# Kernel optimization log

Hardware: AMD Instinct MI355X
Metric: run time of the kernel (lower is better)

Reference implementation:

```python
import jax, jax.numpy as jnp
import numpy as np

N_NODES = 50000
N_EDGES = 800000
IN_DIM = 96
HID = 96
OUT_DIM = 32
N_GRAPHS = 256


def setup_inputs() -> dict:
    key = jax.random.key(0)
    ks = jax.random.split(key, 12)
    x = jax.random.normal(ks[0], (N_NODES, IN_DIM), dtype=jnp.float32)
    edge_index = jax.random.randint(ks[1], (2, N_EDGES), 0, N_NODES, dtype=jnp.int64)
    batch = jnp.sort(jax.random.randint(ks[2], (N_NODES,), 0, N_GRAPHS, dtype=jnp.int64))
    s = 1.0 / np.sqrt(HID)
    W1 = jax.random.normal(ks[3], (IN_DIM, HID), dtype=jnp.float32) * s
    W2 = jax.random.normal(ks[4], (HID, HID), dtype=jnp.float32) * s
    W3 = jax.random.normal(ks[5], (HID, HID), dtype=jnp.float32) * s
    fc_w = jax.random.normal(ks[6], (HID, OUT_DIM), dtype=jnp.float32) * s
    return {
        'x': x, 'edge_index': edge_index, 'batch': batch,
        'W1': W1, 'b1': jnp.zeros((HID,), jnp.float32),
        'W2': W2, 'b2': jnp.zeros((HID,), jnp.float32),
        'W3': W3, 'b3': jnp.zeros((HID,), jnp.float32),
        'fc_w': fc_w, 'fc_b': jnp.zeros((OUT_DIM,), jnp.float32),
    }


def _gcn_conv(h, row, col, norm, W, b, n_nodes):
    # linear transform first (PyG GCNConv), then normalized gather/scatter-add
    h = h @ W                                   # [N, F]
    msg = h[row] * norm[:, None]                # [E+N, F] gather + scale
    out = jax.ops.segment_sum(msg, col, num_segments=n_nodes)
    return out + b


def reference(x, edge_index, batch, W1, b1, W2, b2, W3, b3, fc_w, fc_b):
    n = x.shape[0]
    loop = jnp.arange(n, dtype=edge_index.dtype)
    row = jnp.concatenate([edge_index[0], loop])  # sources (with self-loops)
    col = jnp.concatenate([edge_index[1], loop])  # targets
    # symmetric normalization: deg over targets, norm = d^-1/2[row] * d^-1/2[col]
    deg = jax.ops.segment_sum(jnp.ones_like(col, dtype=x.dtype), col, num_segments=n)
    dis = jnp.where(deg > 0, jax.lax.rsqrt(deg), 0.0)
    norm = dis[row] * dis[col]

    h = jax.nn.relu(_gcn_conv(x, row, col, norm, W1, b1, n))
    h = jax.nn.relu(_gcn_conv(h, row, col, norm, W2, b2, n))
    h = jax.nn.relu(_gcn_conv(h, row, col, norm, W3, b3, n))

    # global_mean_pool over graph ids
    sums = jax.ops.segment_sum(h, batch, num_segments=N_GRAPHS)
    cnts = jax.ops.segment_sum(jnp.ones((n,), h.dtype), batch, num_segments=N_GRAPHS)
    pooled = sums / jnp.maximum(cnts, 1.0)[:, None]
    return pooled @ fc_w + fc_b
```

## Files before the change

kernel.cpp:

```cpp
#include <hip/hip_runtime.h>

#define NN 50000
#define NE 800000
#define F  96
#define FB 48
#define RB4 12
#define OD 32
#define NG 256
#define CAP 64
#define PROWS 21
#define SHARDS 8
#define SHARD_SZ 6250
#define PERSHARD 64
#define NWF 1152
#define RPB 64
#define TPB 256

typedef unsigned int u32;
typedef unsigned short u16;
typedef short short8 __attribute__((ext_vector_type(8)));
typedef float f32x4 __attribute__((ext_vector_type(4)));

static inline size_t align_up(size_t x) { return (x + 255) & ~(size_t)255; }

__device__ inline u32 f2bf_rne(float x) {
    u32 u = __float_as_uint(x);
    return (u + 0x7fffu + ((u >> 16) & 1u)) >> 16;
}
__device__ inline u32 packbf(float a, float b) {
    return f2bf_rne(a) | (f2bf_rne(b) << 16);
}
__device__ inline float bf_lo(u32 u) { return __uint_as_float(u << 16); }
__device__ inline float bf_hi(u32 u) { return __uint_as_float(u & 0xffff0000u); }

__global__ __launch_bounds__(256) void k_pack(const int* __restrict__ src,
                                              const int* __restrict__ tgt,
                                              uint4* __restrict__ ep4) {
    int c = blockIdx.x * 256 + threadIdx.x;
    if (c >= NE / 4) return;
    int4 s4 = reinterpret_cast<const int4*>(src)[c];
    int4 t4 = reinterpret_cast<const int4*>(tgt)[c];
    ep4[c] = make_uint4(((u32)t4.x << 16) | (u32)s4.x, ((u32)t4.y << 16) | (u32)s4.y,
                        ((u32)t4.z << 16) | (u32)s4.z, ((u32)t4.w << 16) | (u32)s4.w);
}

__global__ __launch_bounds__(256) void k_fillb(const uint4* __restrict__ ep4,
                                               int* __restrict__ cnt,
                                               u16* __restrict__ bucket) {
    int shard = blockIdx.x & (SHARDS - 1);
    int sb    = blockIdx.x >> 3;
    int lo    = shard * SHARD_SZ;
    int hi    = lo + SHARD_SZ;
    const int nchunk = NE / 4;
    for (int c = sb * 256 + threadIdx.x; c < nchunk; c += PERSHARD * 256) {
        uint4 p = ep4[c];
        int t0 = p.x >> 16, s0 = p.x & 0xffff;
        int t1 = p.y >> 16, s1 = p.y & 0xffff;
        int t2 = p.z >> 16, s2 = p.z & 0xffff;
        int t3 = p.w >> 16, s3 = p.w & 0xffff;
        if (t0 >= lo && t0 < hi) {
            int q = atomicAdd(&cnt[t0], 1);
            if (q < CAP) bucket[t0 * CAP + q] = (u16)s0;
        }
        if (t1 >= lo && t1 < hi) {
            int q = atomicAdd(&cnt[t1], 1);
            if (q < CAP) bucket[t1 * CAP + q] = (u16)s1;
        }
        if (t2 >= lo && t2 < hi) {
            int q = atomicAdd(&cnt[t2], 1);
            if (q < CAP) bucket[t2 * CAP + q] = (u16)s2;
        }
        if (t3 >= lo && t3 < hi) {
            int q = atomicAdd(&cnt[t3], 1);
            if (q < CAP) bucket[t3 * CAP + q] = (u16)s3;
        }
    }
}

__global__ __launch_bounds__(256) void k_cvt(const float4* __restrict__ x4,
                                             const int* __restrict__ cnt,
                                             float* __restrict__ dis,
                                             uint4* __restrict__ rb4) {
    int i = blockIdx.x * 256 + threadIdx.x;
    if (i >= NN * RB4) return;
    int v   = i / RB4;
    int sub = i - v * RB4;
    float dv = rsqrtf((float)(cnt[v] + 1));
    if (sub == 0) dis[v] = dv;
    float4 f0 = x4[(size_t)i * 2];
    float4 f1 = x4[(size_t)i * 2 + 1];
    rb4[i] = make_uint4(packbf(dv * f0.x, dv * f0.y), packbf(dv * f0.z, dv * f0.w),
                        packbf(dv * f1.x, dv * f1.y), packbf(dv * f1.z, dv * f1.w));
}

__global__ __launch_bounds__(256) void k_wprep3(const float* __restrict__ W1,
                                                const float* __restrict__ W2,
                                                const float* __restrict__ W3,
                                                uint4* __restrict__ wf) {
    int e = blockIdx.x * 256 + threadIdx.x;
    if (e >= 3 * NWF) return;
    int wi = e / NWF;
    int f  = e - wi * NWF;
    const float* W = (wi == 0) ? W1 : ((wi == 1) ? W2 : W3);
    int n  = f & 15;
    int t1 = f >> 4;
    int quad = t1 & 3;
    int t2 = t1 >> 2;
    int kc = t2 % 3;
    int ct = t2 / 3;
    int k  = kc * 32 + quad * 8;
    int col = ct * 16 + n;
    u32 w0 = packbf(W[(k + 0) * F + col], W[(k + 1) * F + col]);
    u32 w1 = packbf(W[(k + 2) * F + col], W[(k + 3) * F + col]);
    u32 w2 = packbf(W[(k + 4) * F + col], W[(k + 5) * F + col]);
    u32 w3 = packbf(W[(k + 6) * F + col], W[(k + 7) * F + col]);
    wf[e] = make_uint4(w0, w1, w2, w3);
}

__global__ __launch_bounds__(TPB) void k_layer(const uint4* __restrict__ rprev,
                                               const uint4* __restrict__ wfragG,
                                               const int* __restrict__ cnt,
                                               const u16* __restrict__ bucket,
                                               const float* __restrict__ dis,
                                               const float* __restrict__ bias,
                                               const int last,
                                               u16* __restrict__ rnext) {
    __shared__ uint4 atile[RPB * 13];
    int tid = threadIdx.x;
    int r0 = blockIdx.x * RPB;

    const u32* hb = reinterpret_cast<const u32*>(rprev);

#pragma unroll
    for (int it = 0; it < 3; ++it) {
        int slot = it * TPB + tid;
        int ln  = slot / 12;
        int sub = slot - ln * 12;
        int v = r0 + ln;
        uint4 res = make_uint4(0u, 0u, 0u, 0u);
        if (v < NN) {
            int co = sub * 4;
            uint4 hv = *reinterpret_cast<const uint4*>(&hb[(size_t)v * FB + co]);
            float a0 = bf_lo(hv.x), a1 = bf_hi(hv.x);
            float a2 = bf_lo(hv.y), a3 = bf_hi(hv.y);
            float a4 = bf_lo(hv.z), a5 = bf_hi(hv.z);
            float a6 = bf_lo(hv.w), a7 = bf_hi(hv.w);

            int deg = cnt[v];
            if (deg > CAP) deg = CAP;
            const u16* bkt = &bucket[v * CAP];
            int e = 0;
            for (; e + 7 < deg; e += 8) {
                uint4 b8 = *reinterpret_cast<const uint4*>(&bkt[e]);
                int s0 = b8.x & 0xffff, s1 = b8.x >> 16;
                int s2 = b8.y & 0xffff, s3 = b8.y >> 16;
                int s4 = b8.z & 0xffff, s5 = b8.z >> 16;
                int s6 = b8.w & 0xffff, s7 = b8.w >> 16;
                uint4 g0 = *reinterpret_cast<const uint4*>(&hb[(size_t)s0 * FB + co]);
                uint4 g1 = *reinterpret_cast<const uint4*>(&hb[(size_t)s1 * FB + co]);
                uint4 g2 = *reinterpret_cast<const uint4*>(&hb[(size_t)s2 * FB + co]);
                uint4 g3 = *reinterpret_cast<const uint4*>(&hb[(size_t)s3 * FB + co]);
                uint4 g4 = *reinterpret_cast<const uint4*>(&hb[(size_t)s4 * FB + co]);
                uint4 g5 = *reinterpret_cast<const uint4*>(&hb[(size_t)s5 * FB + co]);
                uint4 g6 = *reinterpret_cast<const uint4*>(&hb[(size_t)s6 * FB + co]);
                uint4 g7 = *reinterpret_cast<const uint4*>(&hb[(size_t)s7 * FB + co]);
                a0 += bf_lo(g0.x) + bf_lo(g1.x) + bf_lo(g2.x) + bf_lo(g3.x)
                    + bf_lo(g4.x) + bf_lo(g5.x) + bf_lo(g6.x) + bf_lo(g7.x);
                a1 += bf_hi(g0.x) + bf_hi(g1.x) + bf_hi(g2.x) + bf_hi(g3.x)
                    + bf_hi(g4.x) + bf_hi(g5.x) + bf_hi(g6.x) + bf_hi(g7.x);
                a2 += bf_lo(g0.y) + bf_lo(g1.y) + bf_lo(g2.y) + bf_lo(g3.y)
                    + bf_lo(g4.y) + bf_lo(g5.y) + bf_lo(g6.y) + bf_lo(g7.y);
                a3 += bf_hi(g0.y) + bf_hi(g1.y) + bf_hi(g2.y) + bf_hi(g3.y)
                    + bf_hi(g4.y) + bf_hi(g5.y) + bf_hi(g6.y) + bf_hi(g7.y);
                a4 += bf_lo(g0.z) + bf_lo(g1.z) + bf_lo(g2.z) + bf_lo(g3.z)
                    + bf_lo(g4.z) + bf_lo(g5.z) + bf_lo(g6.z) + bf_lo(g7.z);
                a5 += bf_hi(g0.z) + bf_hi(g1.z) + bf_hi(g2.z) + bf_hi(g3.z)
                    + bf_hi(g4.z) + bf_hi(g5.z) + bf_hi(g6.z) + bf_hi(g7.z);
                a6 += bf_lo(g0.w) + bf_lo(g1.w) + bf_lo(g2.w) + bf_lo(g3.w)
                    + bf_lo(g4.w) + bf_lo(g5.w) + bf_lo(g6.w) + bf_lo(g7.w);
                a7 += bf_hi(g0.w) + bf_hi(g1.w) + bf_hi(g2.w) + bf_hi(g3.w)
                    + bf_hi(g4.w) + bf_hi(g5.w) + bf_hi(g6.w) + bf_hi(g7.w);
            }
            for (; e + 3 < deg; e += 4) {
                uint2 b4 = *reinterpret_cast<const uint2*>(&bkt[e]);
                int s0 = b4.x & 0xffff, s1 = b4.x >> 16;
                int s2 = b4.y & 0xffff, s3 = b4.y >> 16;
                uint4 g0 = *reinterpret_cast<const uint4*>(&hb[(size_t)s0 * FB + co]);
                uint4 g1 = *reinterpret_cast<const uint4*>(&hb[(size_t)s1 * FB + co]);
                uint4 g2 = *reinterpret_cast<const uint4*>(&hb[(size_t)s2 * FB + co]);
                uint4 g3 = *reinterpret_cast<const uint4*>(&hb[(size_t)s3 * FB + co]);
                a0 += bf_lo(g0.x) + bf_lo(g1.x) + bf_lo(g2.x) + bf_lo(g3.x);
                a1 += bf_hi(g0.x) + bf_hi(g1.x) + bf_hi(g2.x) + bf_hi(g3.x);
                a2 += bf_lo(g0.y) + bf_lo(g1.y) + bf_lo(g2.y) + bf_lo(g3.y);
                a3 += bf_hi(g0.y) + bf_hi(g1.y) + bf_hi(g2.y) + bf_hi(g3.y);
                a4 += bf_lo(g0.z) + bf_lo(g1.z) + bf_lo(g2.z) + bf_lo(g3.z);
                a5 += bf_hi(g0.z) + bf_hi(g1.z) + bf_hi(g2.z) + bf_hi(g3.z);
                a6 += bf_lo(g0.w) + bf_lo(g1.w) + bf_lo(g2.w) + bf_lo(g3.w);
                a7 += bf_hi(g0.w) + bf_hi(g1.w) + bf_hi(g2.w) + bf_hi(g3.w);
            }
            for (; e < deg; ++e) {
                int s = bkt[e];
                uint4 g = *reinterpret_cast<const uint4*>(&hb[(size_t)s * FB + co]);
                a0 += bf_lo(g.x); a1 += bf_hi(g.x);
                a2 += bf_lo(g.y); a3 += bf_hi(g.y);
                a4 += bf_lo(g.z); a5 += bf_hi(g.z);
                a6 += bf_lo(g.w); a7 += bf_hi(g.w);
            }
            float dv = dis[v];
            res = make_uint4(packbf(dv * a0, dv * a1), packbf(dv * a2, dv * a3),
                             packbf(dv * a4, dv * a5), packbf(dv * a6, dv * a7));
        }
        atile[ln * 13 + sub] = res;
    }
    __syncthreads();

    int wave = tid >> 6;
    int lane = tid & 63;
    int m    = lane & 15;
    int quad = lane >> 4;
    int arow = wave * 16 + m;

    short8 a0 = *reinterpret_cast<const short8*>(&atile[arow * 13 + 0 * 4 + quad]);
    short8 a1 = *reinterpret_cast<const short8*>(&atile[arow * 13 + 1 * 4 + quad]);
    short8 a2 = *reinterpret_cast<const short8*>(&atile[arow * 13 + 2 * 4 + quad]);

    f32x4 acc[6];
#pragma unroll
    for (int ct = 0; ct < 6; ++ct) acc[ct] = (f32x4)(0.0f);
#pragma unroll
    for (int ct = 0; ct < 6; ++ct) {
        short8 b0 = *reinterpret_cast<const short8*>(&wfragG[((ct * 3 + 0) * 4 + quad) * 16 + m]);
        short8 b1 = *reinterpret_cast<const short8*>(&wfragG[((ct * 3 + 1) * 4 + quad) * 16 + m]);
        short8 b2 = *reinterpret_cast<const short8*>(&wfragG[((ct * 3 + 2) * 4 + quad) * 16 + m]);
        acc[ct] = __builtin_amdgcn_mfma_f32_16x16x32_bf16(a0, b0, acc[ct], 0, 0, 0);
        acc[ct] = __builtin_amdgcn_mfma_f32_16x16x32_bf16(a1, b1, acc[ct], 0, 0, 0);
        acc[ct] = __builtin_amdgcn_mfma_f32_16x16x32_bf16(a2, b2, acc[ct], 0, 0, 0);
    }

    int rbase = r0 + wave * 16 + quad * 4;
    float dr[4];
#pragma unroll
    for (int r = 0; r < 4; ++r) {
        int row = rbase + r;
        dr[r] = (row < NN) ? (last ? 1.0f : dis[row]) : 0.0f;
    }
#pragma unroll
    for (int ct = 0; ct < 6; ++ct) {
        float bb = bias[ct * 16 + m];
#pragma unroll
        for (int r = 0; r < 4; ++r) {
            int row = rbase + r;
            if (row < NN) {
                float h = fmaxf(acc[ct][r] + bb, 0.0f);
                rnext[(size_t)row * F + ct * 16 + m] = (u16)f2bf_rne(h * dr[r]);
            }
        }
    }
}

__device__ inline int lower_bound_i(const int* __restrict__ a, int n, int key) {
    int lo = 0, hi = n;
    while (lo < hi) {
        int mid = (lo + hi) >> 1;
        if (a[mid] < key) lo = mid + 1; else hi = mid;
    }
    return lo;
}

__global__ __launch_bounds__(512) void k_poolfc(const uint2* __restrict__ hb2,
                                                const int* __restrict__ batch,
                                                const float* __restrict__ fcw,
                                                const float* __restrict__ fcb,
                                                float* __restrict__ out) {
    __shared__ int range[2];
    __shared__ float4 part[PROWS][24];
    __shared__ float pl[F];
    int g = blockIdx.x;
    int t = threadIdx.x;
    if (t == 0) range[0] = lower_bound_i(batch, NN, g);
    if (t == 1) range[1] = lower_bound_i(batch, NN, g + 1);
    __syncthreads();
    int lo = range[0], hi = range[1];
    int row = t / 24;
    int sub = t - row * 24;
    if (row < PROWS) {
        float4 acc = make_float4(0.f, 0.f, 0.f, 0.f);
        for (int v = lo + row; v < hi; v += PROWS) {
            uint2 xv = hb2[(size_t)v * 24 + sub];
            acc.x += bf_lo(xv.x); acc.y += bf_hi(xv.x);
            acc.z += bf_lo(xv.y); acc.w += bf_hi(xv.y);
        }
        part[row][sub] = acc;
    }
    __syncthreads();
    if (t < 24) {
        float4 s = part[0][t];
        for (int r = 1; r < PROWS; ++r) {
            float4 p = part[r][t];
            s.x += p.x; s.y += p.y; s.z += p.z; s.w += p.w;
        }
        float inv = 1.0f / fmaxf((float)(hi - lo), 1.0f);
        pl[t * 4 + 0] = s.x * inv;
        pl[t * 4 + 1] = s.y * inv;
        pl[t * 4 + 2] = s.z * inv;
        pl[t * 4 + 3] = s.w * inv;
    }
    __syncthreads();
    if (t < OD) {
        float acc = 0.0f;
        for (int f = 0; f < F; ++f) acc += pl[f] * fcw[f * OD + t];
        out[g * OD + t] = acc + fcb[t];
    }
}

extern "C" void kernel_launch(void* const* d_in, const int* in_sizes, int n_in,
                              void* d_out, int out_size, void* d_ws, size_t ws_size,
                              hipStream_t stream) {
    (void)in_sizes; (void)n_in; (void)out_size; (void)ws_size;
    const float* x    = (const float*)d_in[0];
    const int*   ei   = (const int*)d_in[1];
    const int*   batc = (const int*)d_in[2];
    const float* W1   = (const float*)d_in[3];
    const float* b1   = (const float*)d_in[4];
    const float* W2   = (const float*)d_in[5];
    const float* b2   = (const float*)d_in[6];
    const float* W3   = (const float*)d_in[7];
    const float* b3   = (const float*)d_in[8];
    const float* fcw  = (const float*)d_in[9];
    const float* fcb  = (const float*)d_in[10];
    float* out = (float*)d_out;

    const int* src = ei;
    const int* tgt = ei + NE;

    char* ws = (char*)d_ws;
    int*    cnt    = (int*)ws;    ws += align_up((size_t)NN * 4);
    float*  dis    = (float*)ws;  ws += align_up((size_t)NN * 4);
    u16*    bucket = (u16*)ws;    ws += align_up((size_t)NN * CAP * 2);
    u32*    ep     = (u32*)ws;    ws += align_up((size_t)NE * 4);
    u32*    rA     = (u32*)ws;    ws += align_up((size_t)NN * FB * 4);
    u32*    rB     = (u32*)ws;    ws += align_up((size_t)NN * FB * 4);
    uint4*  wfrag3 = (uint4*)ws;  ws += align_up((size_t)3 * NWF * 16);

    const int B = 256;
    const int cvt_grid   = (NN * RB4 + B - 1) / B;
    const int wprep_grid = (3 * NWF + B - 1) / B;
    const int pack_grid  = (NE / 4 + B - 1) / B;
    const int layer_grid = (NN + RPB - 1) / RPB;

    (void)hipMemsetAsync(cnt, 0, (size_t)NN * 4, stream);
    k_pack  <<<pack_grid, B, 0, stream>>>(src, tgt, (uint4*)ep);
    k_fillb <<<SHARDS * PERSHARD, B, 0, stream>>>((const uint4*)ep, cnt, bucket);
    k_wprep3<<<wprep_grid, B, 0, stream>>>(W1, W2, W3, wfrag3);
    k_cvt   <<<cvt_grid, B, 0, stream>>>((const float4*)x, cnt, dis, (uint4*)rA);

    k_layer<<<layer_grid, TPB, 0, stream>>>((const uint4*)rA, wfrag3 + 0 * NWF,
                                            cnt, bucket, dis, b1, 0, (u16*)rB);
    k_layer<<<layer_grid, TPB, 0, stream>>>((const uint4*)rB, wfrag3 + 1 * NWF,
                                            cnt, bucket, dis, b2, 0, (u16*)rA);
    k_layer<<<layer_grid, TPB, 0, stream>>>((const uint4*)rA, wfrag3 + 2 * NWF,
                                            cnt, bucket, dis, b3, 1, (u16*)rB);

    k_poolfc<<<NG, 512, 0, stream>>>((const uint2*)rB, batc, fcw, fcb, out);
}
```

Before: 242.5 us.

## Split fused layer kernel into separate aggregation and MFMA matmul kernels

Replaces the fused per-layer kernel (gather-aggregate into LDS, then MFMA against the weights) with two kernels: a flat gather kernel writing bf16 aggregates to a global scratch buffer, and a matmul kernel that reads them back for the MFMA step. This is meant to decouple the irregular gather from the matmul and raise occupancy for the gather (launch bounds 256,4, no LDS), avoiding the barrier and LDS footprint that limited the fused version. In exchange it adds an extra global write and read of an N x 96 bf16 buffer per layer plus three more kernel launches.

```diff
diff --git a/kernel.cpp b/kernel.cpp
--- a/kernel.cpp
+++ b/kernel.cpp
@@ -14,7 +14,7 @@
 #define PERSHARD 64
 #define NWF 1152
 #define RPB 64
-#define TPB 256
+#define ASLOTS (NN * 12)
 
 typedef unsigned int u32;
 typedef unsigned short u16;
@@ -117,112 +117,111 @@
     wf[e] = make_uint4(w0, w1, w2, w3);
 }
 
-__global__ __launch_bounds__(TPB) void k_layer(const uint4* __restrict__ rprev,
-                                               const uint4* __restrict__ wfragG,
-                                               const int* __restrict__ cnt,
-                                               const u16* __restrict__ bucket,
-                                               const float* __restrict__ dis,
-                                               const float* __restrict__ bias,
-                                               const int last,
-                                               u16* __restrict__ rnext) {
-    __shared__ uint4 atile[RPB * 13];
-    int tid = threadIdx.x;
-    int r0 = blockIdx.x * RPB;
-
+__global__ __launch_bounds__(256, 4) void k_agg(const uint4* __restrict__ rprev,
+                                                const int* __restrict__ cnt,
+                                                const u16* __restrict__ bucket,
+                                                const float* __restrict__ dis,
+                                                uint4* __restrict__ aggb) {
+    int slot = blockIdx.x * 256 + threadIdx.x;
+    if (slot >= ASLOTS) return;
+    int v   = slot / 12;
+    int sub = slot - v * 12;
+    int co  = sub * 4;
     const u32* hb = reinterpret_cast<const u32*>(rprev);
 
-#pragma unroll
-    for (int it = 0; it < 3; ++it) {
-        int slot = it * TPB + tid;
-        int ln  = slot / 12;
-        int sub = slot - ln * 12;
-        int v = r0 + ln;
-        uint4 res = make_uint4(0u, 0u, 0u, 0u);
-        if (v < NN) {
-            int co = sub * 4;
-            uint4 hv = *reinterpret_cast<const uint4*>(&hb[(size_t)v * FB + co]);
-            float a0 = bf_lo(hv.x), a1 = bf_hi(hv.x);
-            float a2 = bf_lo(hv.y), a3 = bf_hi(hv.y);
-            float a4 = bf_lo(hv.z), a5 = bf_hi(hv.z);
-            float a6 = bf_lo(hv.w), a7 = bf_hi(hv.w);
-
-            int deg = cnt[v];
-            if (deg > CAP) deg = CAP;
-            const u16* bkt = &bucket[v * CAP];
-            int e = 0;
-            for (; e + 7 < deg; e += 8) {
-                uint4 b8 = *reinterpret_cast<const uint4*>(&bkt[e]);
-                int s0 = b8.x & 0xffff, s1 = b8.x >> 16;
-                int s2 = b8.y & 0xffff, s3 = b8.y >> 16;
-                int s4 = b8.z & 0xffff, s5 = b8.z >> 16;
-                int s6 = b8.w & 0xffff, s7 = b8.w >> 16;
-                uint4 g0 = *reinterpret_cast<const uint4*>(&hb[(size_t)s0 * FB + co]);
-                uint4 g1 = *reinterpret_cast<const uint4*>(&hb[(size_t)s1 * FB + co]);
-                uint4 g2 = *reinterpret_cast<const uint4*>(&hb[(size_t)s2 * FB + co]);
-                uint4 g3 = *reinterpret_cast<const uint4*>(&hb[(size_t)s3 * FB + co]);
-                uint4 g4 = *reinterpret_cast<const uint4*>(&hb[(size_t)s4 * FB + co]);
-                uint4 g5 = *reinterpret_cast<const uint4*>(&hb[(size_t)s5 * FB + co]);
-                uint4 g6 = *reinterpret_cast<const uint4*>(&hb[(size_t)s6 * FB + co]);
-                uint4 g7 = *reinterpret_cast<const uint4*>(&hb[(size_t)s7 * FB + co]);
-                a0 += bf_lo(g0.x) + bf_lo(g1.x) + bf_lo(g2.x) + bf_lo(g3.x)
-                    + bf_lo(g4.x) + bf_lo(g5.x) + bf_lo(g6.x) + bf_lo(g7.x);
-                a1 += bf_hi(g0.x) + bf_hi(g1.x) + bf_hi(g2.x) + bf_hi(g3.x)
-                    + bf_hi(g4.x) + bf_hi(g5.x) + bf_hi(g6.x) + bf_hi(g7.x);
-                a2 += bf_lo(g0.y) + bf_lo(g1.y) + bf_lo(g2.y) + bf_lo(g3.y)
-                    + bf_lo(g4.y) + bf_lo(g5.y) + bf_lo(g6.y) + bf_lo(g7.y);
-                a3 += bf_hi(g0.y) + bf_hi(g1.y) + bf_hi(g2.y) + bf_hi(g3.y)
-                    + bf_hi(g4.y) + bf_hi(g5.y) + bf_hi(g6.y) + bf_hi(g7.y);
-                a4 += bf_lo(g0.z) + bf_lo(g1.z) + bf_lo(g2.z) + bf_lo(g3.z)
-                    + bf_lo(g4.z) + bf_lo(g5.z) + bf_lo(g6.z) + bf_lo(g7.z);
-                a5 += bf_hi(g0.z) + bf_hi(g1.z) + bf_hi(g2.z) + bf_hi(g3.z)
-                    + bf_hi(g4.z) + bf_hi(g5.z) + bf_hi(g6.z) + bf_hi(g7.z);
-                a6 += bf_lo(g0.w) + bf_lo(g1.w) + bf_lo(g2.w) + bf_lo(g3.w)
-                    + bf_lo(g4.w) + bf_lo(g5.w) + bf_lo(g6.w) + bf_lo(g7.w);
-                a7 += bf_hi(g0.w) + bf_hi(g1.w) + bf_hi(g2.w) + bf_hi(g3.w)
-                    + bf_hi(g4.w) + bf_hi(g5.w) + bf_hi(g6.w) + bf_hi(g7.w);
-            }
-            for (; e + 3 < deg; e += 4) {
-                uint2 b4 = *reinterpret_cast<const uint2*>(&bkt[e]);
-                int s0 = b4.x & 0xffff, s1 = b4.x >> 16;
-                int s2 = b4.y & 0xffff, s3 = b4.y >> 16;
-                uint4 g0 = *reinterpret_cast<const uint4*>(&hb[(size_t)s0 * FB + co]);
-                uint4 g1 = *reinterpret_cast<const uint4*>(&hb[(size_t)s1 * FB + co]);
-                uint4 g2 = *reinterpret_cast<const uint4*>(&hb[(size_t)s2 * FB + co]);
-                uint4 g3 = *reinterpret_cast<const uint4*>(&hb[(size_t)s3 * FB + co]);
-                a0 += bf_lo(g0.x) + bf_lo(g1.x) + bf_lo(g2.x) + bf_lo(g3.x);
-                a1 += bf_hi(g0.x) + bf_hi(g1.x) + bf_hi(g2.x) + bf_hi(g3.x);
-                a2 += bf_lo(g0.y) + bf_lo(g1.y) + bf_lo(g2.y) + bf_lo(g3.y);
-                a3 += bf_hi(g0.y) + bf_hi(g1.y) + bf_hi(g2.y) + bf_hi(g3.y);
-                a4 += bf_lo(g0.z) + bf_lo(g1.z) + bf_lo(g2.z) + bf_lo(g3.z);
-                a5 += bf_hi(g0.z) + bf_hi(g1.z) + bf_hi(g2.z) + bf_hi(g3.z);
-                a6 += bf_lo(g0.w) + bf_lo(g1.w) + bf_lo(g2.w) + bf_lo(g3.w);
-                a7 += bf_hi(g0.w) + bf_hi(g1.w) + bf_hi(g2.w) + bf_hi(g3.w);
-            }
-            for (; e < deg; ++e) {
-                int s = bkt[e];
-                uint4 g = *reinterpret_cast<const uint4*>(&hb[(size_t)s * FB + co]);
-                a0 += bf_lo(g.x); a1 += bf_hi(g.x);
-                a2 += bf_lo(g.y); a3 += bf_hi(g.y);
-                a4 += bf_lo(g.z); a5 += bf_hi(g.z);
-                a6 += bf_lo(g.w); a7 += bf_hi(g.w);
-            }
-            float dv = dis[v];
-            res = make_uint4(packbf(dv * a0, dv * a1), packbf(dv * a2, dv * a3),
-                             packbf(dv * a4, dv * a5), packbf(dv * a6, dv * a7));
-        }
-        atile[ln * 13 + sub] = res;
-    }
-    __syncthreads();
-
+    uint4 hv = *reinterpret_cast<const uint4*>(&hb[(size_t)v * FB + co]);
+    float a0 = bf_lo(hv.x), a1 = bf_hi(hv.x);
+    float a2 = bf_lo(hv.y), a3 = bf_hi(hv.y);
+    float a4 = bf_lo(hv.z), a5 = bf_hi(hv.z);
+    float a6 = bf_lo(hv.w), a7 = bf_hi(hv.w);
+
+    int deg = cnt[v];
+    if (deg > CAP) deg = CAP;
+    const u16* bkt = &bucket[v * CAP];
+    int e = 0;
+    for (; e + 7 < deg; e += 8) {
+        uint4 b8 = *reinterpret_cast<const uint4*>(&bkt[e]);
+        int s0 = b8.x & 0xffff, s1 = b8.x >> 16;
+        int s2 = b8.y & 0xffff, s3 = b8.y >> 16;
+        int s4 = b8.z & 0xffff, s5 = b8.z >> 16;
+        int s6 = b8.w & 0xffff, s7 = b8.w >> 16;
+        uint4 g0 = *reinterpret_cast<const uint4*>(&hb[(size_t)s0 * FB + co]);
+        uint4 g1 = *reinterpret_cast<const uint4*>(&hb[(size_t)s1 * FB + co]);
+        uint4 g2 = *reinterpret_cast<const uint4*>(&hb[(size_t)s2 * FB + co]);
+        uint4 g3 = *reinterpret_cast<const uint4*>(&hb[(size_t)s3 * FB + co]);
+        uint4 g4 = *reinterpret_cast<const uint4*>(&hb[(size_t)s4 * FB + co]);
+        uint4 g5 = *reinterpret_cast<const uint4*>(&hb[(size_t)s5 * FB + co]);
+        uint4 g6 = *reinterpret_cast<const uint4*>(&hb[(size_t)s6 * FB + co]);
+        uint4 g7 = *reinterpret_cast<const uint4*>(&hb[(size_t)s7 * FB + co]);
+        a0 += bf_lo(g0.x) + bf_lo(g1.x) + bf_lo(g2.x) + bf_lo(g3.x)
+            + bf_lo(g4.x) + bf_lo(g5.x) + bf_lo(g6.x) + bf_lo(g7.x);
+        a1 += bf_hi(g0.x) + bf_hi(g1.x) + bf_hi(g2.x) + bf_hi(g3.x)
+            + bf_hi(g4.x) + bf_hi(g5.x) + bf_hi(g6.x) + bf_hi(g7.x);
+        a2 += bf_lo(g0.y) + bf_lo(g1.y) + bf_lo(g2.y) + bf_lo(g3.y)
+            + bf_lo(g4.y) + bf_lo(g5.y) + bf_lo(g6.y) + bf_lo(g7.y);
+        a3 += bf_hi(g0.y) + bf_hi(g1.y) + bf_hi(g2.y) + bf_hi(g3.y)
+            + bf_hi(g4.y) + bf_hi(g5.y) + bf_hi(g6.y) + bf_hi(g7.y);
+        a4 += bf_lo(g0.z) + bf_lo(g1.z) + bf_lo(g2.z) + bf_lo(g3.z)
+            + bf_lo(g4.z) + bf_lo(g5.z) + bf_lo(g6.z) + bf_lo(g7.z);
+        a5 += bf_hi(g0.z) + bf_hi(g1.z) + bf_hi(g2.z) + bf_hi(g3.z)
+            + bf_hi(g4.z) + bf_hi(g5.z) + bf_hi(g6.z) + bf_hi(g7.z);
+        a6 += bf_lo(g0.w) + bf_lo(g1.w) + bf_lo(g2.w) + bf_lo(g3.w)
+            + bf_lo(g4.w) + bf_lo(g5.w) + bf_lo(g6.w) + bf_lo(g7.w);
+        a7 += bf_hi(g0.w) + bf_hi(g1.w) + bf_hi(g2.w) + bf_hi(g3.w)
+            + bf_hi(g4.w) + bf_hi(g5.w) + bf_hi(g6.w) + bf_hi(g7.w);
+    }
+    for (; e + 3 < deg; e += 4) {
+        uint2 b4 = *reinterpret_cast<const uint2*>(&bkt[e]);
+        int s0 = b4.x & 0xffff, s1 = b4.x >> 16;
+        int s2 = b4.y & 0xffff, s3 = b4.y >> 16;
+        uint4 g0 = *reinterpret_cast<const uint4*>(&hb[(size_t)s0 * FB + co]);
+        uint4 g1 = *reinterpret_cast<const uint4*>(&hb[(size_t)s1 * FB + co]);
+        uint4 g2 = *reinterpret_cast<const uint4*>(&hb[(size_t)s2 * FB + co]);
+        uint4 g3 = *reinterpret_cast<const uint4*>(&hb[(size_t)s3 * FB + co]);
+        a0 += bf_lo(g0.x) + bf_lo(g1.x) + bf_lo(g2.x) + bf_lo(g3.x);
+        a1 += bf_hi(g0.x) + bf_hi(g1.x) + bf_hi(g2.x) + bf_hi(g3.x);
+        a2 += bf_lo(g0.y) + bf_lo(g1.y) + bf_lo(g2.y) + bf_lo(g3.y);
+        a3 += bf_hi(g0.y) + bf_hi(g1.y) + bf_hi(g2.y) + bf_hi(g3.y);
+        a4 += bf_lo(g0.z) + bf_lo(g1.z) + bf_lo(g2.z) + bf_lo(g3.z);
+        a5 += bf_hi(g0.z) + bf_hi(g1.z) + bf_hi(g2.z) + bf_hi(g3.z);
+        a6 += bf_lo(g0.w) + bf_lo(g1.w) + bf_lo(g2.w) + bf_lo(g3.w);
+        a7 += bf_hi(g0.w) + bf_hi(g1.w) + bf_hi(g2.w) + bf_hi(g3.w);
+    }
+    for (; e < deg; ++e) {
+        int s = bkt[e];
+        uint4 g = *reinterpret_cast<const uint4*>(&hb[(size_t)s * FB + co]);
+        a0 += bf_lo(g.x); a1 += bf_hi(g.x);
+        a2 += bf_lo(g.y); a3 += bf_hi(g.y);
+        a4 += bf_lo(g.z); a5 += bf_hi(g.z);
+        a6 += bf_lo(g.w); a7 += bf_hi(g.w);
+    }
+    float dv = dis[v];
+    aggb[slot] = make_uint4(packbf(dv * a0, dv * a1), packbf(dv * a2, dv * a3),
+                            packbf(dv * a4, dv * a5), packbf(dv * a6, dv * a7));
+}
+
+__global__ __launch_bounds__(256) void k_mm(const uint4* __restrict__ aggb,
+                                            const uint4* __restrict__ wfragG,
+                                            const float* __restrict__ dis,
+                                            const float* __restrict__ bias,
+                                            const int last,
+                                            u16* __restrict__ rnext) {
+    int tid  = threadIdx.x;
+    int r0   = blockIdx.x * RPB;
     int wave = tid >> 6;
     int lane = tid & 63;
     int m    = lane & 15;
     int quad = lane >> 4;
-    int arow = wave * 16 + m;
-
-    short8 a0 = *reinterpret_cast<const short8*>(&atile[arow * 13 + 0 * 4 + quad]);
-    short8 a1 = *reinterpret_cast<const short8*>(&atile[arow * 13 + 1 * 4 + quad]);
-    short8 a2 = *reinterpret_cast<const short8*>(&atile[arow * 13 + 2 * 4 + quad]);
+    int arow = r0 + wave * 16 + m;
+    bool rv  = arow < NN;
+
+    size_t abase = (size_t)arow * 12;
+    short8 a0 = (short8)(short)0, a1 = (short8)(short)0, a2 = (short8)(short)0;
+    if (rv) {
+        a0 = *reinterpret_cast<const short8*>(&aggb[abase + 0 * 4 + quad]);
+        a1 = *reinterpret_cast<const short8*>(&aggb[abase + 1 * 4 + quad]);
+        a2 = *reinterpret_cast<const short8*>(&aggb[abase + 2 * 4 + quad]);
+    }
 
     f32x4 acc[6];
 #pragma unroll
@@ -340,13 +339,15 @@
     u32*    ep     = (u32*)ws;    ws += align_up((size_t)NE * 4);
     u32*    rA     = (u32*)ws;    ws += align_up((size_t)NN * FB * 4);
     u32*    rB     = (u32*)ws;    ws += align_up((size_t)NN * FB * 4);
+    u32*    rC     = (u32*)ws;    ws += align_up((size_t)NN * FB * 4);
     uint4*  wfrag3 = (uint4*)ws;  ws += align_up((size_t)3 * NWF * 16);
 
     const int B = 256;
     const int cvt_grid   = (NN * RB4 + B - 1) / B;
     const int wprep_grid = (3 * NWF + B - 1) / B;
     const int pack_grid  = (NE / 4 + B - 1) / B;
-    const int layer_grid = (NN + RPB - 1) / RPB;
+    const int agg_grid   = (ASLOTS + B - 1) / B;
+    const int mm_grid    = (NN + RPB - 1) / RPB;
 
     (void)hipMemsetAsync(cnt, 0, (size_t)NN * 4, stream);
     k_pack  <<<pack_grid, B, 0, stream>>>(src, tgt, (uint4*)ep);
@@ -354,12 +355,14 @@
     k_wprep3<<<wprep_grid, B, 0, stream>>>(W1, W2, W3, wfrag3);
     k_cvt   <<<cvt_grid, B, 0, stream>>>((const float4*)x, cnt, dis, (uint4*)rA);
 
-    k_layer<<<layer_grid, TPB, 0, stream>>>((const uint4*)rA, wfrag3 + 0 * NWF,
-                                            cnt, bucket, dis, b1, 0, (u16*)rB);
-    k_layer<<<layer_grid, TPB, 0, stream>>>((const uint4*)rB, wfrag3 + 1 * NWF,
-                                            cnt, bucket, dis, b2, 0, (u16*)rA);
-    k_layer<<<layer_grid, TPB, 0, stream>>>((const uint4*)rA, wfrag3 + 2 * NWF,
-                                            cnt, bucket, dis, b3, 1, (u16*)rB);
+    k_agg<<<agg_grid, B, 0, stream>>>((const uint4*)rA, cnt, bucket, dis, (uint4*)rC);
+    k_mm <<<mm_grid, B, 0, stream>>>((const uint4*)rC, wfrag3 + 0 * NWF, dis, b1, 0, (u16*)rB);
+
+    k_agg<<<agg_grid, B, 0, stream>>>((const uint4*)rB, cnt, bucket, dis, (uint4*)rC);
+    k_mm <<<mm_grid, B, 0, stream>>>((const uint4*)rC, wfrag3 + 1 * NWF, dis, b2, 0, (u16*)rA);
+
+    k_agg<<<agg_grid, B, 0, stream>>>((const uint4*)rA, cnt, bucket, dis, (uint4*)rC);
+    k_mm <<<mm_grid, B, 0, stream>>>((const uint4*)rC, wfrag3 + 2 * NWF, dis, b3, 1, (u16*)rB);
 
     k_poolfc<<<NG, 512, 0, stream>>>((const uint2*)rB, batc, fcw, fcb, out);
 }
```

New measurement: 249.8 us. 3.0% more time.

## Process nodes in degree-sorted order and fuse setup kernels

Applied to the files above, without the earlier changes.

Adds a counting sort of nodes by in-degree (a histogram built in the prep kernel plus a scatter kernel that builds a permutation). Each layer block then handles rows through that permutation, so warps gather similar numbers of neighbours and divergence and load imbalance shrink. The memset, edge pack and weight-prep steps are merged into one kernel to cut launches. In exchange it adds a permutation indirection, scattered output writes, and global atomics during the histogram and scatter.

```diff
diff --git a/kernel.cpp b/kernel.cpp
--- a/kernel.cpp
+++ b/kernel.cpp
@@ -33,15 +33,42 @@
 __device__ inline float bf_lo(u32 u) { return __uint_as_float(u << 16); }
 __device__ inline float bf_hi(u32 u) { return __uint_as_float(u & 0xffff0000u); }
 
-__global__ __launch_bounds__(256) void k_pack(const int* __restrict__ src,
-                                              const int* __restrict__ tgt,
-                                              uint4* __restrict__ ep4) {
-    int c = blockIdx.x * 256 + threadIdx.x;
-    if (c >= NE / 4) return;
-    int4 s4 = reinterpret_cast<const int4*>(src)[c];
-    int4 t4 = reinterpret_cast<const int4*>(tgt)[c];
-    ep4[c] = make_uint4(((u32)t4.x << 16) | (u32)s4.x, ((u32)t4.y << 16) | (u32)s4.y,
-                        ((u32)t4.z << 16) | (u32)s4.z, ((u32)t4.w << 16) | (u32)s4.w);
+__global__ __launch_bounds__(256) void k_prep1(const int* __restrict__ src,
+                                               const int* __restrict__ tgt,
+                                               const float* __restrict__ W1,
+                                               const float* __restrict__ W2,
+                                               const float* __restrict__ W3,
+                                               uint4* __restrict__ wf,
+                                               int* __restrict__ cnt,
+                                               int* __restrict__ histcur,
+                                               uint4* __restrict__ ep4) {
+    int g = blockIdx.x * 256 + threadIdx.x;
+    if (g < NN) cnt[g] = 0;
+    if (g < 2 * (CAP + 1)) histcur[g] = 0;
+    if (g < NE / 4) {
+        int4 s4 = reinterpret_cast<const int4*>(src)[g];
+        int4 t4 = reinterpret_cast<const int4*>(tgt)[g];
+        ep4[g] = make_uint4(((u32)t4.x << 16) | (u32)s4.x, ((u32)t4.y << 16) | (u32)s4.y,
+                            ((u32)t4.z << 16) | (u32)s4.z, ((u32)t4.w << 16) | (u32)s4.w);
+    }
+    if (g < 3 * NWF) {
+        int wi = g / NWF;
+        int f  = g - wi * NWF;
+        const float* W = (wi == 0) ? W1 : ((wi == 1) ? W2 : W3);
+        int n  = f & 15;
+        int t1 = f >> 4;
+        int quad = t1 & 3;
+        int t2 = t1 >> 2;
+        int kc = t2 % 3;
+        int ct = t2 / 3;
+        int k  = kc * 32 + quad * 8;
+        int col = ct * 16 + n;
+        u32 w0 = packbf(W[(k + 0) * F + col], W[(k + 1) * F + col]);
+        u32 w1 = packbf(W[(k + 2) * F + col], W[(k + 3) * F + col]);
+        u32 w2 = packbf(W[(k + 4) * F + col], W[(k + 5) * F + col]);
+        u32 w3 = packbf(W[(k + 6) * F + col], W[(k + 7) * F + col]);
+        wf[g] = make_uint4(w0, w1, w2, w3);
+    }
 }
 
 __global__ __launch_bounds__(256) void k_fillb(const uint4* __restrict__ ep4,
@@ -77,44 +104,46 @@
     }
 }
 
-__global__ __launch_bounds__(256) void k_cvt(const float4* __restrict__ x4,
-                                             const int* __restrict__ cnt,
-                                             float* __restrict__ dis,
-                                             uint4* __restrict__ rb4) {
+__global__ __launch_bounds__(256) void k_prep2(const float4* __restrict__ x4,
+                                               const int* __restrict__ cnt,
+                                               float* __restrict__ dis,
+                                               uint4* __restrict__ rb4,
+                                               int* __restrict__ histcur) {
     int i = blockIdx.x * 256 + threadIdx.x;
     if (i >= NN * RB4) return;
     int v   = i / RB4;
     int sub = i - v * RB4;
     float dv = rsqrtf((float)(cnt[v] + 1));
-    if (sub == 0) dis[v] = dv;
+    if (sub == 0) {
+        dis[v] = dv;
+        int d = cnt[v];
+        if (d > CAP) d = CAP;
+        atomicAdd(&histcur[d], 1);
+    }
     float4 f0 = x4[(size_t)i * 2];
     float4 f1 = x4[(size_t)i * 2 + 1];
     rb4[i] = make_uint4(packbf(dv * f0.x, dv * f0.y), packbf(dv * f0.z, dv * f0.w),
                         packbf(dv * f1.x, dv * f1.y), packbf(dv * f1.z, dv * f1.w));
 }
 
-__global__ __launch_bounds__(256) void k_wprep3(const float* __restrict__ W1,
-                                                const float* __restrict__ W2,
-                                                const float* __restrict__ W3,
-                                                uint4* __restrict__ wf) {
-    int e = blockIdx.x * 256 + threadIdx.x;
-    if (e >= 3 * NWF) return;
-    int wi = e / NWF;
-    int f  = e - wi * NWF;
-    const float* W = (wi == 0) ? W1 : ((wi == 1) ? W2 : W3);
-    int n  = f & 15;
-    int t1 = f >> 4;
-    int quad = t1 & 3;
-    int t2 = t1 >> 2;
-    int kc = t2 % 3;
-    int ct = t2 / 3;
-    int k  = kc * 32 + quad * 8;
-    int col = ct * 16 + n;
-    u32 w0 = packbf(W[(k + 0) * F + col], W[(k + 1) * F + col]);
-    u32 w1 = packbf(W[(k + 2) * F + col], W[(k + 3) * F + col]);
-    u32 w2 = packbf(W[(k + 4) * F + col], W[(k + 5) * F + col]);
-    u32 w3 = packbf(W[(k + 6) * F + col], W[(k + 7) * F + col]);
-    wf[e] = make_uint4(w0, w1, w2, w3);
+__global__ __launch_bounds__(256) void k_scatter(const int* __restrict__ cnt,
+                                                 int* __restrict__ histcur,
+                                                 int* __restrict__ perm) {
+    __shared__ int sstart[CAP + 1];
+    int t = threadIdx.x;
+    if (t <= CAP) {
+        int s = 0;
+        for (int d2 = CAP; d2 > t; --d2) s += histcur[d2];
+        sstart[t] = s;
+    }
+    __syncthreads();
+    int v = blockIdx.x * 256 + t;
+    if (v < NN) {
+        int d = cnt[v];
+        if (d > CAP) d = CAP;
+        int pos = sstart[d] + atomicAdd(&histcur[(CAP + 1) + d], 1);
+        perm[pos] = v;
+    }
 }
 
 __global__ __launch_bounds__(TPB) void k_layer(const uint4* __restrict__ rprev,
@@ -123,6 +152,7 @@
                                                const u16* __restrict__ bucket,
                                                const float* __restrict__ dis,
                                                const float* __restrict__ bias,
+                                               const int* __restrict__ perm,
                                                const int last,
                                                u16* __restrict__ rnext) {
     __shared__ uint4 atile[RPB * 13];
@@ -136,9 +166,10 @@
         int slot = it * TPB + tid;
         int ln  = slot / 12;
         int sub = slot - ln * 12;
-        int v = r0 + ln;
+        int idx = r0 + ln;
         uint4 res = make_uint4(0u, 0u, 0u, 0u);
-        if (v < NN) {
+        if (idx < NN) {
+            int v = perm[idx];
             int co = sub * 4;
             uint4 hv = *reinterpret_cast<const uint4*>(&hb[(size_t)v * FB + co]);
             float a0 = bf_lo(hv.x), a1 = bf_hi(hv.x);
@@ -239,10 +270,17 @@
 
     int rbase = r0 + wave * 16 + quad * 4;
     float dr[4];
+    int prow[4];
 #pragma unroll
     for (int r = 0; r < 4; ++r) {
         int row = rbase + r;
-        dr[r] = (row < NN) ? (last ? 1.0f : dis[row]) : 0.0f;
+        if (row < NN) {
+            prow[r] = perm[row];
+            dr[r] = last ? 1.0f : dis[prow[r]];
+        } else {
+            prow[r] = 0;
+            dr[r] = 0.0f;
+        }
     }
 #pragma unroll
     for (int ct = 0; ct < 6; ++ct) {
@@ -252,7 +290,7 @@
             int row = rbase + r;
             if (row < NN) {
                 float h = fmaxf(acc[ct][r] + bb, 0.0f);
-                rnext[(size_t)row * F + ct * 16 + m] = (u16)f2bf_rne(h * dr[r]);
+                rnext[(size_t)prow[r] * F + ct * 16 + m] = (u16)f2bf_rne(h * dr[r]);
             }
         }
     }
@@ -341,25 +379,28 @@
     u32*    rA     = (u32*)ws;    ws += align_up((size_t)NN * FB * 4);
     u32*    rB     = (u32*)ws;    ws += align_up((size_t)NN * FB * 4);
     uint4*  wfrag3 = (uint4*)ws;  ws += align_up((size_t)3 * NWF * 16);
+    int*    perm   = (int*)ws;    ws += align_up((size_t)NN * 4);
+    int*    histc  = (int*)ws;    ws += align_up((size_t)2 * (CAP + 1) * 4);
 
     const int B = 256;
-    const int cvt_grid   = (NN * RB4 + B - 1) / B;
-    const int wprep_grid = (3 * NWF + B - 1) / B;
-    const int pack_grid  = (NE / 4 + B - 1) / B;
+    const int prep1_grid = (NE / 4 + B - 1) / B;
+    const int prep2_grid = (NN * RB4 + B - 1) / B;
+    const int scat_grid  = (NN + B - 1) / B;
     const int layer_grid = (NN + RPB - 1) / RPB;
 
-    (void)hipMemsetAsync(cnt, 0, (size_t)NN * 4, stream);
-    k_pack  <<<pack_grid, B, 0, stream>>>(src, tgt, (uint4*)ep);
-    k_fillb <<<SHARDS * PERSHARD, B, 0, stream>>>((const uint4*)ep, cnt, bucket);
-    k_wprep3<<<wprep_grid, B, 0, stream>>>(W1, W2, W3, wfrag3);
-    k_cvt   <<<cvt_grid, B, 0, stream>>>((const float4*)x, cnt, dis, (uint4*)rA);
+    k_prep1  <<<prep1_grid, B, 0, stream>>>(src, tgt, W1, W2, W3, wfrag3,
+                                            cnt, histc, (uint4*)ep);
+    k_fillb  <<<SHARDS * PERSHARD, B, 0, stream>>>((const uint4*)ep, cnt, bucket);
+    k_prep2  <<<prep2_grid, B, 0, stream>>>((const float4*)x, cnt, dis,
+                                            (uint4*)rA, histc);
+    k_scatter<<<scat_grid, B, 0, stream>>>(cnt, histc, perm);
 
     k_layer<<<layer_grid, TPB, 0, stream>>>((const uint4*)rA, wfrag3 + 0 * NWF,
-                                            cnt, bucket, dis, b1, 0, (u16*)rB);
+                                            cnt, bucket, dis, b1, perm, 0, (u16*)rB);
     k_layer<<<layer_grid, TPB, 0, stream>>>((const uint4*)rB, wfrag3 + 1 * NWF,
-                                            cnt, bucket, dis, b2, 0, (u16*)rA);
+                                            cnt, bucket, dis, b2, perm, 0, (u16*)rA);
     k_layer<<<layer_grid, TPB, 0, stream>>>((const uint4*)rA, wfrag3 + 2 * NWF,
-                                            cnt, bucket, dis, b3, 1, (u16*)rB);
+                                            cnt, bucket, dis, b3, perm, 1, (u16*)rB);
 
     k_poolfc<<<NG, 512, 0, stream>>>((const uint2*)rB, batc, fcw, fcb, out);
 }
```

Result: slower. 534.9 us (+120.6%).
